# Kernel tuning notes

Hardware: AMD Instinct MI355X
Metric: run time of the kernel (lower is better)

The kernel has to match this reference:

```python
import jax, jax.numpy as jnp
import numpy as np

N_QUBITS = 10
DEPTH = 6


def _ry(theta):
    # RY(theta) = [[cos(t/2), -sin(t/2)], [sin(t/2), cos(t/2)]]
    c = jnp.cos(theta / 2)
    s = jnp.sin(theta / 2)
    return jnp.stack([jnp.stack([c, -s]), jnp.stack([s, c])]).astype(jnp.complex64)


def _rot(phi, theta, omega):
    # PennyLane Rot(phi, theta, omega) = RZ(omega) RY(theta) RZ(phi)
    c = jnp.cos(theta / 2)
    s = jnp.sin(theta / 2)
    ep = jnp.exp(-0.5j * (phi + omega).astype(jnp.complex64))
    em = jnp.exp(-0.5j * (phi - omega).astype(jnp.complex64))
    return jnp.stack([
        jnp.stack([ep * c, -jnp.conj(em) * s]),
        jnp.stack([em * s, jnp.conj(ep) * c]),
    ])


def _apply_1q(psi, U, w):
    # psi: (2,)*n statevector; apply 2x2 unitary U on qubit axis w
    psi = jnp.tensordot(U, psi, axes=([1], [w]))
    return jnp.moveaxis(psi, 0, w)


def _apply_cnot(psi, c, t):
    # flip target axis t on the control=1 slice of axis c
    psi = jnp.moveaxis(psi, (c, t), (0, 1))
    psi = jnp.concatenate([psi[:1], psi[1:, ::-1]], axis=0)
    return jnp.moveaxis(psi, (0, 1), (c, t))


def _circuit(angles, weights):
    """RY encoding + StronglyEntanglingLayers + PauliZ expvals. angles: (n,), weights: (depth, n, 3)."""
    n = N_QUBITS
    psi = jnp.zeros((2,) * n, jnp.complex64).at[(0,) * n].set(1.0)
    for i in range(n):
        psi = _apply_1q(psi, _ry(angles[i]), i)
    for l in range(DEPTH):
        for i in range(n):
            psi = _apply_1q(psi, _rot(weights[l, i, 0], weights[l, i, 1], weights[l, i, 2]), i)
        r = (l % (n - 1)) + 1  # default StronglyEntanglingLayers range schedule
        for i in range(n):
            psi = _apply_cnot(psi, i, (i + r) % n)
    p = psi.real ** 2 + psi.imag ** 2  # probabilities, shape (2,)*n
    exps = []
    for i in range(n):
        pm = jnp.moveaxis(p, i, 0).reshape(2, -1).sum(axis=1)
        exps.append(pm[0] - pm[1])  # <Z_i>
    return jnp.stack(exps)


def setup_inputs() -> dict:
    key = jax.random.key(0)
    ks = jax.random.split(key, 5)
    B, F, C = 8192, 1024, 10
    x = jax.random.normal(ks[0], (B, F), jnp.float32)
    W_proj = jax.random.normal(ks[1], (N_QUBITS, F), jnp.float32) / np.sqrt(F).astype(np.float32)
    weights = 0.01 * jax.random.normal(ks[2], (DEPTH, N_QUBITS, 3), jnp.float32)
    W_out = jax.random.normal(ks[3], (C, N_QUBITS), jnp.float32) / np.sqrt(N_QUBITS).astype(np.float32)
    b_out = 0.01 * jax.random.normal(ks[4], (C,), jnp.float32)
    return {"x": x, "W_proj": W_proj, "weights": weights, "W_out": W_out, "b_out": b_out}


def reference(x, W_proj, weights, W_out, b_out):
    # classical projection + angle encoding
    angles = jnp.tanh(x @ W_proj.T) * jnp.float32(np.pi / 2)  # (B, n_qubits)
    # batched exact statevector simulation of the VQC
    q = jax.vmap(_circuit, in_axes=(0, None))(angles, weights)  # (B, n_qubits)
    return q @ W_out.T + b_out  # (B, num_classes)
```

## Files before the change

kernel.cpp:

```cpp
#include <hip/hip_runtime.h>
#include <math.h>
#include <stdint.h>

#define NQ 10
#define DEPTH 6

typedef _Float16 f16x8 __attribute__((ext_vector_type(8)));
typedef float f32x4 __attribute__((ext_vector_type(4)));

typedef __attribute__((address_space(3))) unsigned int lds_u32;
typedef const __attribute__((address_space(1))) unsigned int glb_u32;

__device__ __forceinline__ void async_load16(const unsigned short* g, unsigned short* l) {
    __builtin_amdgcn_global_load_lds((glb_u32*)g, (lds_u32*)l, 16, 0, 0);
}

template <int M>
__device__ __forceinline__ float lane_xor(float v) {
    if constexpr (M == 1) {
        int r = __builtin_amdgcn_update_dpp(
            __builtin_bit_cast(int, v), __builtin_bit_cast(int, v),
            0xB1, 0xF, 0xF, false);
        return __builtin_bit_cast(float, r);
    } else if constexpr (M == 2) {
        int r = __builtin_amdgcn_update_dpp(
            __builtin_bit_cast(int, v), __builtin_bit_cast(int, v),
            0x4E, 0xF, 0xF, false);
        return __builtin_bit_cast(float, r);
    } else if constexpr (M == 4) {
        return __builtin_bit_cast(float,
            __builtin_amdgcn_ds_swizzle(__builtin_bit_cast(int, v), 0x101F));
    } else if constexpr (M == 8) {
        return __builtin_bit_cast(float,
            __builtin_amdgcn_ds_swizzle(__builtin_bit_cast(int, v), 0x201F));
    } else if constexpr (M == 16) {
        return __builtin_bit_cast(float,
            __builtin_amdgcn_ds_swizzle(__builtin_bit_cast(int, v), 0x401F));
    } else {
        return __shfl_xor(v, 32, 64);
    }
}

__device__ __forceinline__ void compute_gate(const float* __restrict__ weights,
                                             int idx, float* __restrict__ g) {
    float phi   = weights[idx * 3 + 0];
    float theta = weights[idx * 3 + 1];
    float omega = weights[idx * 3 + 2];
    float c = cosf(0.5f * theta), s = sinf(0.5f * theta);
    float ap = -0.5f * (phi + omega);
    float am = -0.5f * (phi - omega);
    float epr = cosf(ap), epi = sinf(ap);
    float emr = cosf(am), emi = sinf(am);
    g[0] =  epr * c;  g[1] =  epi * c;
    g[2] = -emr * s;  g[3] =  emi * s;
    g[4] =  emr * s;  g[5] =  emi * s;
    g[6] =  epr * c;  g[7] = -epi * c;
}

__global__ void prep_gates_kernel(const float* __restrict__ weights,
                                  float* __restrict__ gmat) {
    int idx = blockIdx.x * blockDim.x + threadIdx.x;
    if (idx >= DEPTH * NQ) return;
    compute_gate(weights, idx, gmat + idx * 8);
}

template <int Q>
__device__ __forceinline__ void rotT_gate(float (&ar)[16], float (&ai)[16], int lane,
                                          const float* __restrict__ g) {
    float u00r = g[0], u00i = g[1];
    float u01r = g[4], u01i = g[5];
    float u10r = g[2], u10i = g[3];
    float u11r = g[6], u11i = g[7];
    if constexpr (Q < 4) {
#pragma unroll
        for (int j = 0; j < 16; ++j) {
            if ((j >> Q) & 1) continue;
            int j1 = j | (1 << Q);
            float a0r = ar[j],  a0i = ai[j];
            float a1r = ar[j1], a1i = ai[j1];
            ar[j]  = u00r*a0r - u00i*a0i + u01r*a1r - u01i*a1i;
            ai[j]  = u00r*a0i + u00i*a0r + u01r*a1i + u01i*a1r;
            ar[j1] = u10r*a0r - u10i*a0i + u11r*a1r - u11i*a1i;
            ai[j1] = u10r*a0i + u10i*a0r + u11r*a1i + u11i*a1r;
        }
    } else {
        constexpr int M = 1 << (Q - 4);
        bool hi = (lane >> (Q - 4)) & 1;
        float car = hi ? u11r : u00r, cai = hi ? u11i : u00i;
        float cbr = hi ? u10r : u01r, cbi = hi ? u10i : u01i;
        float pr[16], pi[16];
#pragma unroll
        for (int j = 0; j < 16; ++j) pr[j] = lane_xor<M>(ar[j]);
#pragma unroll
        for (int j = 0; j < 16; ++j) pi[j] = lane_xor<M>(ai[j]);
#pragma unroll
        for (int j = 0; j < 16; ++j) {
            float mr = ar[j], mi = ai[j];
            ar[j] = car*mr - cai*mi + cbr*pr[j] - cbi*pi[j];
            ai[j] = car*mi + cai*mr + cbr*pi[j] + cbi*pr[j];
        }
    }
}

__device__ __forceinline__ void rotT_layer(float (&ar)[16], float (&ai)[16], int lane,
                                           const float* __restrict__ gl) {
    rotT_gate<0>(ar, ai, lane, gl + 0);
    rotT_gate<1>(ar, ai, lane, gl + 8);
    rotT_gate<2>(ar, ai, lane, gl + 16);
    rotT_gate<3>(ar, ai, lane, gl + 24);
    rotT_gate<4>(ar, ai, lane, gl + 32);
    rotT_gate<5>(ar, ai, lane, gl + 40);
    rotT_gate<6>(ar, ai, lane, gl + 48);
    rotT_gate<7>(ar, ai, lane, gl + 56);
    rotT_gate<8>(ar, ai, lane, gl + 64);
    rotT_gate<9>(ar, ai, lane, gl + 72);
}

template <int C, int T>
__device__ __forceinline__ void cnot_t(float (&ar)[16], float (&ai)[16], int lane) {
    if constexpr (C < 4 && T < 4) {
#pragma unroll
        for (int j = 0; j < 16; ++j) {
            if (((j >> C) & 1) && !((j >> T) & 1)) {
                int j1 = j | (1 << T);
                float tr = ar[j]; ar[j] = ar[j1]; ar[j1] = tr;
                float ti = ai[j]; ai[j] = ai[j1]; ai[j1] = ti;
            }
        }
    } else if constexpr (C < 4) {
        constexpr int M = 1 << (T - 4);
        float pr[16], pi[16];
#pragma unroll
        for (int j = 0; j < 16; ++j)
            if ((j >> C) & 1) pr[j] = lane_xor<M>(ar[j]);
#pragma unroll
        for (int j = 0; j < 16; ++j)
            if ((j >> C) & 1) pi[j] = lane_xor<M>(ai[j]);
#pragma unroll
        for (int j = 0; j < 16; ++j)
            if ((j >> C) & 1) { ar[j] = pr[j]; ai[j] = pi[j]; }
    } else if constexpr (T < 4) {
        bool cb = (lane >> (C - 4)) & 1;
#pragma unroll
        for (int j = 0; j < 16; ++j) {
            if (!((j >> T) & 1)) {
                int j1 = j | (1 << T);
                float lr = ar[j], li = ai[j], hr = ar[j1], hi2 = ai[j1];
                ar[j]  = cb ? hr : lr;  ai[j]  = cb ? hi2 : li;
                ar[j1] = cb ? lr : hr;  ai[j1] = cb ? li : hi2;
            }
        }
    } else {
        constexpr int M = 1 << (T - 4);
        bool cb = (lane >> (C - 4)) & 1;
        float pr[16], pi[16];
#pragma unroll
        for (int j = 0; j < 16; ++j) pr[j] = lane_xor<M>(ar[j]);
#pragma unroll
        for (int j = 0; j < 16; ++j) pi[j] = lane_xor<M>(ai[j]);
#pragma unroll
        for (int j = 0; j < 16; ++j) {
            ar[j] = cb ? pr[j] : ar[j];
            ai[j] = cb ? pi[j] : ai[j];
        }
    }
}

template <int R, int I>
__device__ __forceinline__ void cnot_ring_rev_t(float (&ar)[16], float (&ai)[16], int lane) {
    cnot_t<I, (I + R) % NQ>(ar, ai, lane);
    if constexpr (I > 0) cnot_ring_rev_t<R, I - 1>(ar, ai, lane);
}

__device__ __forceinline__ void run_circuit_T(float (&ar)[16], float (&ai)[16],
                                              const float* __restrict__ gmat, int lane) {
    for (int l = DEPTH - 1; l >= 0; --l) {
        switch (l) {
            case 0: cnot_ring_rev_t<1, NQ - 1>(ar, ai, lane); break;
            case 1: cnot_ring_rev_t<2, NQ - 1>(ar, ai, lane); break;
            case 2: cnot_ring_rev_t<3, NQ - 1>(ar, ai, lane); break;
            case 3: cnot_ring_rev_t<4, NQ - 1>(ar, ai, lane); break;
            case 4: cnot_ring_rev_t<5, NQ - 1>(ar, ai, lane); break;
            default: cnot_ring_rev_t<6, NQ - 1>(ar, ai, lane); break;
        }
        rotT_layer(ar, ai, lane, gmat + l * (NQ * 8));
    }
}

__device__ __forceinline__ float wave_sum(float v) {
    v += lane_xor<1>(v);
    v += lane_xor<2>(v);
    v += lane_xor<4>(v);
    v += lane_xor<8>(v);
    v += lane_xor<16>(v);
    v += lane_xor<32>(v);
    return v;
}

__device__ __forceinline__ void apply_1q_local(
    float (&ar)[16], float (&ai)[16], int q,
    float u00r, float u00i, float u01r, float u01i,
    float u10r, float u10i, float u11r, float u11i) {
#pragma unroll
    for (int j = 0; j < 16; ++j) {
        if ((j >> q) & 1) continue;
        int j1 = j | (1 << q);
        float a0r = ar[j],  a0i = ai[j];
        float a1r = ar[j1], a1i = ai[j1];
        ar[j]  = u00r*a0r - u00i*a0i + u01r*a1r - u01i*a1i;
        ai[j]  = u00r*a0i + u00i*a0r + u01r*a1i + u01i*a1r;
        ar[j1] = u10r*a0r - u10i*a0i + u11r*a1r - u11i*a1i;
        ai[j1] = u10r*a0i + u10i*a0r + u11r*a1i + u11i*a1r;
    }
}

__device__ __forceinline__ void apply_1q_lane(
    float (&ar)[16], float (&ai)[16], int q, int lane,
    float u00r, float u00i, float u01r, float u01i,
    float u10r, float u10i, float u11r, float u11i) {
    int  m  = 1 << (q - 4);
    bool hi = (lane >> (q - 4)) & 1;
    float car = hi ? u11r : u00r, cai = hi ? u11i : u00i;
    float cbr = hi ? u10r : u01r, cbi = hi ? u10i : u01i;
    float pr[16], pi[16];
#pragma unroll
    for (int j = 0; j < 16; ++j) pr[j] = __shfl_xor(ar[j], m, 64);
#pragma unroll
    for (int j = 0; j < 16; ++j) pi[j] = __shfl_xor(ai[j], m, 64);
#pragma unroll
    for (int j = 0; j < 16; ++j) {
        float mr = ar[j], mi = ai[j];
        ar[j] = car*mr - cai*mi + cbr*pr[j] - cbi*pi[j];
        ai[j] = car*mi + cai*mr + cbr*pi[j] + cbi*pr[j];
    }
}

__device__ __forceinline__ void cnot_gate(
    float (&ar)[16], float (&ai)[16], int c, int t, int lane) {
    if (c < 4 && t < 4) {
#pragma unroll
        for (int j = 0; j < 16; ++j) {
            if (((j >> c) & 1) && !((j >> t) & 1)) {
                int j1 = j | (1 << t);
                float tr = ar[j]; ar[j] = ar[j1]; ar[j1] = tr;
                float ti = ai[j]; ai[j] = ai[j1]; ai[j1] = ti;
            }
        }
    } else if (c < 4) {
        int m = 1 << (t - 4);
        float pr[16], pi[16];
#pragma unroll
        for (int j = 0; j < 16; ++j)
            if ((j >> c) & 1) pr[j] = __shfl_xor(ar[j], m, 64);
#pragma unroll
        for (int j = 0; j < 16; ++j)
            if ((j >> c) & 1) pi[j] = __shfl_xor(ai[j], m, 64);
#pragma unroll
        for (int j = 0; j < 16; ++j)
            if ((j >> c) & 1) { ar[j] = pr[j]; ai[j] = pi[j]; }
    } else if (t < 4) {
        bool cb = (lane >> (c - 4)) & 1;
#pragma unroll
        for (int j = 0; j < 16; ++j) {
            if (!((j >> t) & 1)) {
                int j1 = j | (1 << t);
                float lr = ar[j], li = ai[j], hr = ar[j1], hi2 = ai[j1];
                ar[j]  = cb ? hr : lr;  ai[j]  = cb ? hi2 : li;
                ar[j1] = cb ? lr : hr;  ai[j1] = cb ? li : hi2;
            }
        }
    } else {
        int  m  = 1 << (t - 4);
        bool cb = (lane >> (c - 4)) & 1;
        float pr[16], pi[16];
#pragma unroll
        for (int j = 0; j < 16; ++j) pr[j] = __shfl_xor(ar[j], m, 64);
#pragma unroll
        for (int j = 0; j < 16; ++j) pi[j] = __shfl_xor(ai[j], m, 64);
#pragma unroll
        for (int j = 0; j < 16; ++j) {
            ar[j] = cb ? pr[j] : ar[j];
            ai[j] = cb ? pi[j] : ai[j];
        }
    }
}

template <int R>
__device__ __forceinline__ void cnot_ring(float (&ar)[16], float (&ai)[16], int lane) {
#pragma unroll
    for (int i = 0; i < NQ; ++i) cnot_gate(ar, ai, i, (i + R) % NQ, lane);
}

__device__ __forceinline__ void run_circuit(float (&ar)[16], float (&ai)[16],
                                            const float* __restrict__ gmat, int lane) {
    for (int l = 0; l < DEPTH; ++l) {
        const float* gl = gmat + l * (NQ * 8);
#pragma unroll
        for (int i = 0; i < NQ; ++i) {
            const float* g = gl + i * 8;
            float u00r = g[0], u00i = g[1], u01r = g[2], u01i = g[3];
            float u10r = g[4], u10i = g[5], u11r = g[6], u11i = g[7];
            if (i < 4)
                apply_1q_local(ar, ai, i, u00r,u00i,u01r,u01i,u10r,u10i,u11r,u11i);
            else
                apply_1q_lane(ar, ai, i, lane, u00r,u00i,u01r,u01i,u10r,u10i,u11r,u11i);
        }
        switch (l) {
            case 0: cnot_ring<1>(ar, ai, lane); break;
            case 1: cnot_ring<2>(ar, ai, lane); break;
            case 2: cnot_ring<3>(ar, ai, lane); break;
            case 3: cnot_ring<4>(ar, ai, lane); break;
            case 4: cnot_ring<5>(ar, ai, lane); break;
            default: cnot_ring<6>(ar, ai, lane); break;
        }
    }
}

__device__ __forceinline__ void proj_v_body(
    const float* __restrict__ x, const float* __restrict__ Wproj,
    _Float16* __restrict__ V, int b, int lane) {
    const float4* xb4 = (const float4*)(x + (size_t)b * 1024);
    const float4* W4  = (const float4*)Wproj;
    float acc[NQ];
#pragma unroll
    for (int q = 0; q < NQ; ++q) acc[q] = 0.f;
#pragma unroll
    for (int k4 = 0; k4 < 4; ++k4) {
        float4 xv = xb4[k4 * 64 + lane];
#pragma unroll
        for (int q = 0; q < NQ; ++q) {
            float4 wv = W4[q * 256 + k4 * 64 + lane];
            acc[q] = fmaf(xv.x, wv.x, acc[q]);
            acc[q] = fmaf(xv.y, wv.y, acc[q]);
            acc[q] = fmaf(xv.z, wv.z, acc[q]);
            acc[q] = fmaf(xv.w, wv.w, acc[q]);
        }
    }
#pragma unroll
    for (int q = 0; q < NQ; ++q) acc[q] = wave_sum(acc[q]);

    float cq[NQ], sq[NQ];
#pragma unroll
    for (int q = 0; q < NQ; ++q) {
        float e  = __expf(2.f * acc[q]);
        float th = 1.f - __fdividef(2.f, e + 1.f);
        float ha = th * 0.785398163397448310f;
        cq[q] = __cosf(ha);
        sq[q] = __sinf(ha);
    }
    float laneprod = 1.f;
#pragma unroll
    for (int q = 4; q < NQ; ++q)
        laneprod *= ((lane >> (q - 4)) & 1) ? sq[q] : cq[q];

    unsigned int buf[8];
#pragma unroll
    for (int jj = 0; jj < 8; ++jj) {
        unsigned short h2[2];
#pragma unroll
        for (int c = 0; c < 2; ++c) {
            int j = jj * 2 + c;
            float p = laneprod;
#pragma unroll
            for (int q = 0; q < 4; ++q) p *= ((j >> q) & 1) ? sq[q] : cq[q];
            h2[c] = __builtin_bit_cast(unsigned short, (_Float16)p);
        }
        buf[jj] = (unsigned int)h2[0] | ((unsigned int)h2[1] << 16);
    }
    uint4* dst = (uint4*)(V + (size_t)b * 1024 + 16 * lane);
    uint4 v0; v0.x = buf[0]; v0.y = buf[1]; v0.z = buf[2]; v0.w = buf[3];
    uint4 v1; v1.x = buf[4]; v1.y = buf[5]; v1.z = buf[6]; v1.w = buf[7];
    dst[0] = v0; dst[1] = v1;
}

__global__ __launch_bounds__(256) void basis_proj_kernel(
    const float* __restrict__ weights, _Float16* __restrict__ Bt,
    const float* __restrict__ x, const float* __restrict__ Wproj,
    _Float16* __restrict__ V, int B) {
    __shared__ float gmat_s[DEPTH * NQ * 8];
    int tid  = threadIdx.x;
    int lane = tid & 63;
    int w    = tid >> 6;

    if (blockIdx.x < 256) {
        if (tid < DEPTH * NQ) compute_gate(weights, tid, gmat_s + tid * 8);
        __syncthreads();

        int g = blockIdx.x * 4 + w;
        float ar[16], ai[16];
#pragma unroll
        for (int jj = 0; jj < 16; ++jj) {
            ar[jj] = (lane == (g >> 4) && jj == (g & 15)) ? 1.f : 0.f;
            ai[jj] = 0.f;
        }
        run_circuit_T(ar, ai, gmat_s, lane);

        unsigned int bufr[8], bufi[8];
#pragma unroll
        for (int jj = 0; jj < 8; ++jj) {
            unsigned short r0 = __builtin_bit_cast(unsigned short, (_Float16)ar[2*jj]);
            unsigned short r1 = __builtin_bit_cast(unsigned short, (_Float16)ar[2*jj+1]);
            unsigned short i0 = __builtin_bit_cast(unsigned short, (_Float16)ai[2*jj]);
            unsigned short i1 = __builtin_bit_cast(unsigned short, (_Float16)ai[2*jj+1]);
            bufr[jj] = (unsigned int)r0 | ((unsigned int)r1 << 16);
            bufi[jj] = (unsigned int)i0 | ((unsigned int)i1 << 16);
        }
        uint4* dre = (uint4*)((unsigned short*)Bt + (size_t)(2*g)     * 1024 + 16 * lane);
        uint4* dim = (uint4*)((unsigned short*)Bt + (size_t)(2*g + 1) * 1024 + 16 * lane);
        uint4 v;
        v.x = bufr[0]; v.y = bufr[1]; v.z = bufr[2]; v.w = bufr[3]; dre[0] = v;
        v.x = bufr[4]; v.y = bufr[5]; v.z = bufr[6]; v.w = bufr[7]; dre[1] = v;
        v.x = bufi[0]; v.y = bufi[1]; v.z = bufi[2]; v.w = bufi[3]; dim[0] = v;
        v.x = bufi[4]; v.y = bufi[5]; v.z = bufi[6]; v.w = bufi[7]; dim[1] = v;
    } else {
        int b = (blockIdx.x - 256) * 4 + w;
        if (b < B) proj_v_body(x, Wproj, V, b, lane);
    }
}

#define STG(dst_, src_, kt_) do {                                                   \
    _Pragma("unroll")                                                               \
    for (int s_ = 0; s_ < 2; ++s_) {                                                \
        async_load16(src_ + (size_t)(s_ * 128 + srow) * 1024 + (kt_) * 32 + scg * 8,\
                     dst_ + s_ * 4096 + w * 512);                                   \
    }                                                                               \
} while (0)

__global__ __launch_bounds__(512, 2) void gemm_fused_kernel(
    const unsigned short* __restrict__ A,
    const unsigned short* __restrict__ Bt,
    float* __restrict__ Zpart) {
    __shared__ __align__(16) unsigned short lds_s[4 * 16384];
    int tid  = threadIdx.x;
    int lane = tid & 63;
    int w    = tid >> 6;
    int wm   = w >> 2;
    int wn   = w & 3;
    int by   = blockIdx.x & 7;
    int bx   = blockIdx.x >> 3;
    int m0   = bx * 256;
    int n0   = by * 256;
    int quad = lane >> 4;
    int lrow = lane & 15;
    int csw  = (quad ^ ((lrow >> 1) & 3)) * 8;
    int srow = tid >> 2;
    int scg  = (tid & 3) ^ ((srow >> 1) & 3);
    const unsigned short* Abase = A  + (size_t)m0 * 1024;
    const unsigned short* Bbase = Bt + (size_t)n0 * 1024;

    f32x4 acc[8][4];
#pragma unroll
    for (int mi = 0; mi < 8; ++mi)
#pragma unroll
        for (int ni = 0; ni < 4; ++ni)
            acc[mi][ni] = (f32x4){0.f, 0.f, 0.f, 0.f};

    STG(lds_s + 0 * 16384,        Abase, 0);
    STG(lds_s + 0 * 16384 + 8192, Bbase, 0);
    STG(lds_s + 1 * 16384,        Abase, 1);
    STG(lds_s + 1 * 16384 + 8192, Bbase, 1);
    STG(lds_s + 2 * 16384,        Abase, 2);
    STG(lds_s + 2 * 16384 + 8192, Bbase, 2);
    asm volatile("s_waitcnt vmcnt(8)" ::: "memory");
    __builtin_amdgcn_s_barrier();

    int rowA = wm * 128 + lrow;
    int rowB = wn * 64  + lrow;

    for (int t = 0; t < 32; ++t) {
        const unsigned short* bufA = lds_s + (t & 3) * 16384;
        const unsigned short* bufB = bufA + 8192;
        unsigned short* nbuf = lds_s + ((t + 3) & 3) * 16384;
        f16x8 af[4], bf[4];
#pragma unroll
        for (int i = 0; i < 4; ++i)
            af[i] = *(const f16x8*)(bufA + (rowA + i * 16) * 32 + csw);
#pragma unroll
        for (int i = 0; i < 4; ++i)
            bf[i] = *(const f16x8*)(bufB + (rowB + i * 16) * 32 + csw);
        if (t < 29) STG(nbuf, Abase, t + 3);
        __builtin_amdgcn_s_barrier();
        asm volatile("s_waitcnt lgkmcnt(0)" ::: "memory");
        __builtin_amdgcn_sched_barrier(0);
        __builtin_amdgcn_s_setprio(1);
#pragma unroll
        for (int mi = 0; mi < 4; ++mi)
#pragma unroll
            for (int ni = 0; ni < 4; ++ni)
                acc[mi][ni] = __builtin_amdgcn_mfma_f32_16x16x32_f16(
                    af[mi], bf[ni], acc[mi][ni], 0, 0, 0);
        __builtin_amdgcn_s_setprio(0);
        __builtin_amdgcn_s_barrier();
#pragma unroll
        for (int i = 0; i < 4; ++i)
            af[i] = *(const f16x8*)(bufA + (rowA + 64 + i * 16) * 32 + csw);
        if (t < 29) {
            STG(nbuf + 8192, Bbase, t + 3);
            asm volatile("s_waitcnt vmcnt(8)" ::: "memory");
        } else {
            asm volatile("s_waitcnt vmcnt(0)" ::: "memory");
        }
        __builtin_amdgcn_s_barrier();
        asm volatile("s_waitcnt lgkmcnt(0)" ::: "memory");
        __builtin_amdgcn_sched_barrier(0);
        __builtin_amdgcn_s_setprio(1);
#pragma unroll
        for (int mi = 0; mi < 4; ++mi)
#pragma unroll
            for (int ni = 0; ni < 4; ++ni)
                acc[mi + 4][ni] = __builtin_amdgcn_mfma_f32_16x16x32_f16(
                    af[mi], bf[ni], acc[mi + 4][ni], 0, 0, 0);
        __builtin_amdgcn_s_setprio(0);
        __builtin_amdgcn_s_barrier();
    }

    float* Zs = (float*)lds_s;
    int nbl  = wn >> 1;
    int half = wn & 1;
#pragma unroll
    for (int mi = 0; mi < 8; ++mi) {
#pragma unroll
        for (int r = 0; r < 4; ++r) {
            float p0 = acc[mi][0][r] * acc[mi][0][r];
            float p1 = acc[mi][1][r] * acc[mi][1][r];
            float p2 = acc[mi][2][r] * acc[mi][2][r];
            float p3 = acc[mi][3][r] * acc[mi][3][r];
            float t0 = (p0 + p1) + (p2 + p3);
            float t3 = (p0 - p1) + (p2 - p3);
            float t4 = (p0 + p1) - (p2 + p3);
            t0 += lane_xor<1>(t0);
            t3 += lane_xor<1>(t3);
            t4 += lane_xor<1>(t4);
            float u2 = lane_xor<2>(t0);
            float ap = t0 + u2;
            float am = (lane & 2) ? u2 - t0 : t0 - u2;
            t3 += lane_xor<2>(t3);
            t4 += lane_xor<2>(t4);
            float u4  = lane_xor<4>(ap);
            float bpp = ap + u4;
            float bpm = (lane & 4) ? u4 - ap : ap - u4;
            float bmp = am + lane_xor<4>(am);
            t3 += lane_xor<4>(t3);
            t4 += lane_xor<4>(t4);
            float u8 = lane_xor<8>(bpp);
            float T  = bpp + u8;
            float Z2 = (lane & 8) ? u8 - bpp : bpp - u8;
            float Z1 = bpm + lane_xor<8>(bpm);
            float Z0 = bmp + lane_xor<8>(bmp);
            t3 += lane_xor<8>(t3);
            t4 += lane_xor<8>(t4);
            if (lrow == 0) {
                int row = wm * 128 + mi * 16 + quad * 4 + r;
                float* z = Zs + ((size_t)(nbl * 2 + half) * 256 + row) * 9;
                z[0] = T;  z[1] = Z0; z[2] = Z1; z[3] = Z2;
                z[4] = t3; z[5] = t4;
            }
        }
    }
    __syncthreads();
    {
        int row  = tid >> 1, part = tid & 1;
#pragma unroll
        for (int nb = 0; nb < 2; ++nb) {
            const float* za = Zs + ((size_t)(nb * 2 + 0) * 256 + row) * 9;
            const float* zb = Zs + ((size_t)(nb * 2 + 1) * 256 + row) * 9;
            float o[4];
            if (part == 0) {
                o[0] = za[0] + zb[0];
                o[1] = za[1] + zb[1];
                o[2] = za[2] + zb[2];
                o[3] = za[3] + zb[3];
            } else {
                o[0] = za[4] + zb[4];
                o[1] = za[5] + zb[5];
                o[2] = za[0] - zb[0];
                o[3] = 0.f;
            }
            float4 v = {o[0], o[1], o[2], o[3]};
            *(float4*)(Zpart + ((size_t)(m0 + row) * 16 + (by * 2 + nb)) * 8 + part * 4) = v;
        }
    }
}

__global__ __launch_bounds__(256) void combine_head_kernel(
    const float* __restrict__ Zpart, const float* __restrict__ Wout,
    const float* __restrict__ bout, float* __restrict__ out, int B) {
    int lane = threadIdx.x & 63;
    int wid  = threadIdx.x >> 6;
    int b    = blockIdx.x * 4 + wid;
    if (b >= B) return;

    float z[8];
    if (lane < 16) {
        const float4* p = (const float4*)(Zpart + ((size_t)b * 16 + lane) * 8);
        float4 a = p[0], c = p[1];
        z[0]=a.x; z[1]=a.y; z[2]=a.z; z[3]=a.w; z[4]=c.x; z[5]=c.y; z[6]=c.z; z[7]=c.w;
    } else {
#pragma unroll
        for (int i = 0; i < 8; ++i) z[i] = 0.f;
    }
    float Zq[NQ];
#pragma unroll
    for (int q = 0; q < 6; ++q) {
        float v = z[q + 1];
        v += lane_xor<1>(v);
        v += lane_xor<2>(v);
        v += lane_xor<4>(v);
        v += lane_xor<8>(v);
        Zq[q] = v;
    }
    {
        float T = z[0];
        float u1 = lane_xor<1>(T);
        float P  = T + u1;
        float M  = (lane & 1) ? u1 - T : T - u1;
        float u2 = lane_xor<2>(P);
        float PP = P + u2;
        float PM = (lane & 2) ? u2 - P : P - u2;
        float MP = M + lane_xor<2>(M);
        float u4  = lane_xor<4>(PP);
        float PPP = PP + u4;
        float PPM = (lane & 4) ? u4 - PP : PP - u4;
        float PMP = PM + lane_xor<4>(PM);
        float MPP = MP + lane_xor<4>(MP);
        float u8 = lane_xor<8>(PPP);
        Zq[9] = (lane & 8) ? u8 - PPP : PPP - u8;
        Zq[8] = PPM + lane_xor<8>(PPM);
        Zq[7] = PMP + lane_xor<8>(PMP);
        Zq[6] = MPP + lane_xor<8>(MPP);
    }
    if (lane < NQ) {
        float o = bout[lane];
#pragma unroll
        for (int q = 0; q < NQ; ++q) o = fmaf(Zq[q], Wout[lane * NQ + q], o);
        out[(size_t)b * NQ + lane] = o;
    }
}

__global__ __launch_bounds__(256) void vqc_kernel(
    const float* __restrict__ x, const float* __restrict__ Wproj,
    const float* __restrict__ gmat, const float* __restrict__ Wout,
    const float* __restrict__ bout, float* __restrict__ out, int B) {
    int lane = threadIdx.x & 63;
    int wid  = threadIdx.x >> 6;
    int b    = blockIdx.x * 4 + wid;
    if (b >= B) return;

    const float* xb = x + (size_t)b * 1024;
    float acc[NQ];
#pragma unroll
    for (int q = 0; q < NQ; ++q) acc[q] = 0.f;
#pragma unroll
    for (int k = 0; k < 16; ++k) {
        float xv = xb[k * 64 + lane];
#pragma unroll
        for (int q = 0; q < NQ; ++q)
            acc[q] = fmaf(xv, Wproj[q * 1024 + k * 64 + lane], acc[q]);
    }
#pragma unroll
    for (int q = 0; q < NQ; ++q) acc[q] = wave_sum(acc[q]);

    float cq[NQ], sq[NQ];
#pragma unroll
    for (int q = 0; q < NQ; ++q) {
        float ang = tanhf(acc[q]) * 1.57079632679489662f;
        cq[q] = cosf(0.5f * ang);
        sq[q] = sinf(0.5f * ang);
    }
    float laneprod = 1.f;
#pragma unroll
    for (int q = 4; q < NQ; ++q)
        laneprod *= ((lane >> (q - 4)) & 1) ? sq[q] : cq[q];
    float ar[16], ai[16];
#pragma unroll
    for (int j = 0; j < 16; ++j) {
        float p = laneprod;
#pragma unroll
        for (int q = 0; q < 4; ++q) p *= ((j >> q) & 1) ? sq[q] : cq[q];
        ar[j] = p; ai[j] = 0.f;
    }
    run_circuit(ar, ai, gmat, lane);

    float T = 0.f, S[4] = {0.f, 0.f, 0.f, 0.f};
#pragma unroll
    for (int j = 0; j < 16; ++j) {
        float p = ar[j] * ar[j] + ai[j] * ai[j];
        T += p;
#pragma unroll
        for (int q = 0; q < 4; ++q) S[q] += ((j >> q) & 1) ? -p : p;
    }
    float Zq[NQ];
#pragma unroll
    for (int q = 0; q < 4; ++q) Zq[q] = S[q];
#pragma unroll
    for (int q = 4; q < NQ; ++q) Zq[q] = ((lane >> (q - 4)) & 1) ? -T : T;
#pragma unroll
    for (int q = 0; q < NQ; ++q) Zq[q] = wave_sum(Zq[q]);
    if (lane < NQ) {
        float o = bout[lane];
#pragma unroll
        for (int q = 0; q < NQ; ++q) o = fmaf(Zq[q], Wout[lane * NQ + q], o);
        out[(size_t)b * NQ + lane] = o;
    }
}

extern "C" void kernel_launch(void* const* d_in, const int* in_sizes, int n_in,
                              void* d_out, int out_size, void* d_ws, size_t ws_size,
                              hipStream_t stream) {
    const float* x       = (const float*)d_in[0];
    const float* Wproj   = (const float*)d_in[1];
    const float* weights = (const float*)d_in[2];
    const float* Wout    = (const float*)d_in[3];
    const float* bout    = (const float*)d_in[4];
    float* out = (float*)d_out;
    int B = in_sizes[0] / 1024;

    char* ws = (char*)d_ws;
    size_t off_Bt = 4096;
    size_t off_V  = off_Bt + (size_t)2048 * 1024 * 2;
    size_t off_Z  = off_V  + (size_t)B * 1024 * 2;
    size_t need   = off_Z  + (size_t)B * 16 * 8 * 4;

    if (ws_size >= need && (B % 256) == 0) {
        _Float16* Bt = (_Float16*)(ws + off_Bt);
        _Float16* V  = (_Float16*)(ws + off_V);
        float*  Zprt = (float*)(ws + off_Z);

        basis_proj_kernel<<<256 + B / 4, 256, 0, stream>>>(weights, Bt, x, Wproj, V, B);
        gemm_fused_kernel<<<(B / 256) * 8, 512, 0, stream>>>(
            (const unsigned short*)V, (const unsigned short*)Bt, Zprt);
        combine_head_kernel<<<B / 4, 256, 0, stream>>>(Zprt, Wout, bout, out, B);
    } else {
        float* gmat = (float*)ws;
        prep_gates_kernel<<<1, 64, 0, stream>>>(weights, gmat);
        vqc_kernel<<<(B + 3) / 4, 256, 0, stream>>>(x, Wproj, gmat, Wout, bout, out, B);
    }
}
```

Measured before the change: 149.6 us.

## Fuse combine/head stage into GEMM epilogue with atomic accumulation into output

Removes the separate combine_head kernel and the Zpart workspace. Each GEMM block now folds its partial per-qubit expectation sums through W_out and atomically adds them into the output, with the bias added by the by==0 blocks. The output is zeroed in the basis/projection kernel, which also moves to 512-thread blocks. This drops one launch and the partial-sum round trip through global memory. The cost is 10 float atomics per row per column block and a non-deterministic summation order.

```diff
diff --git a/kernel.cpp b/kernel.cpp
--- a/kernel.cpp
+++ b/kernel.cpp
@@ -373,20 +373,22 @@
     dst[0] = v0; dst[1] = v1;
 }
 
-__global__ __launch_bounds__(256) void basis_proj_kernel(
+__global__ __launch_bounds__(512) void basis_proj_kernel(
     const float* __restrict__ weights, _Float16* __restrict__ Bt,
     const float* __restrict__ x, const float* __restrict__ Wproj,
-    _Float16* __restrict__ V, int B) {
+    _Float16* __restrict__ V, float* __restrict__ out, int B) {
     __shared__ float gmat_s[DEPTH * NQ * 8];
     int tid  = threadIdx.x;
     int lane = tid & 63;
     int w    = tid >> 6;
 
-    if (blockIdx.x < 256) {
+    if (blockIdx.x < 128) {
+        for (int i = blockIdx.x * 512 + tid; i < B * NQ; i += 128 * 512)
+            out[i] = 0.f;
         if (tid < DEPTH * NQ) compute_gate(weights, tid, gmat_s + tid * 8);
         __syncthreads();
 
-        int g = blockIdx.x * 4 + w;
+        int g = blockIdx.x * 8 + w;
         float ar[16], ai[16];
 #pragma unroll
         for (int jj = 0; jj < 16; ++jj) {
@@ -413,7 +415,7 @@
         v.x = bufi[0]; v.y = bufi[1]; v.z = bufi[2]; v.w = bufi[3]; dim[0] = v;
         v.x = bufi[4]; v.y = bufi[5]; v.z = bufi[6]; v.w = bufi[7]; dim[1] = v;
     } else {
-        int b = (blockIdx.x - 256) * 4 + w;
+        int b = (int)(blockIdx.x - 128) * 8 + w;
         if (b < B) proj_v_body(x, Wproj, V, b, lane);
     }
 }
@@ -429,7 +431,9 @@
 __global__ __launch_bounds__(512, 2) void gemm_fused_kernel(
     const unsigned short* __restrict__ A,
     const unsigned short* __restrict__ Bt,
-    float* __restrict__ Zpart) {
+    const float* __restrict__ Wout,
+    const float* __restrict__ bout,
+    float* __restrict__ out) {
     __shared__ __align__(16) unsigned short lds_s[4 * 16384];
     int tid  = threadIdx.x;
     int lane = tid & 63;
@@ -558,82 +562,37 @@
         }
     }
     __syncthreads();
-    {
-        int row  = tid >> 1, part = tid & 1;
-#pragma unroll
-        for (int nb = 0; nb < 2; ++nb) {
-            const float* za = Zs + ((size_t)(nb * 2 + 0) * 256 + row) * 9;
-            const float* zb = Zs + ((size_t)(nb * 2 + 1) * 256 + row) * 9;
-            float o[4];
-            if (part == 0) {
-                o[0] = za[0] + zb[0];
-                o[1] = za[1] + zb[1];
-                o[2] = za[2] + zb[2];
-                o[3] = za[3] + zb[3];
-            } else {
-                o[0] = za[4] + zb[4];
-                o[1] = za[5] + zb[5];
-                o[2] = za[0] - zb[0];
-                o[3] = 0.f;
-            }
-            float4 v = {o[0], o[1], o[2], o[3]};
-            *(float4*)(Zpart + ((size_t)(m0 + row) * 16 + (by * 2 + nb)) * 8 + part * 4) = v;
-        }
-    }
-}
-
-__global__ __launch_bounds__(256) void combine_head_kernel(
-    const float* __restrict__ Zpart, const float* __restrict__ Wout,
-    const float* __restrict__ bout, float* __restrict__ out, int B) {
-    int lane = threadIdx.x & 63;
-    int wid  = threadIdx.x >> 6;
-    int b    = blockIdx.x * 4 + wid;
-    if (b >= B) return;
-
-    float z[8];
-    if (lane < 16) {
-        const float4* p = (const float4*)(Zpart + ((size_t)b * 16 + lane) * 8);
-        float4 a = p[0], c = p[1];
-        z[0]=a.x; z[1]=a.y; z[2]=a.z; z[3]=a.w; z[4]=c.x; z[5]=c.y; z[6]=c.z; z[7]=c.w;
-    } else {
-#pragma unroll
-        for (int i = 0; i < 8; ++i) z[i] = 0.f;
-    }
-    float Zq[NQ];
-#pragma unroll
-    for (int q = 0; q < 6; ++q) {
-        float v = z[q + 1];
-        v += lane_xor<1>(v);
-        v += lane_xor<2>(v);
-        v += lane_xor<4>(v);
-        v += lane_xor<8>(v);
-        Zq[q] = v;
-    }
-    {
-        float T = z[0];
-        float u1 = lane_xor<1>(T);
-        float P  = T + u1;
-        float M  = (lane & 1) ? u1 - T : T - u1;
-        float u2 = lane_xor<2>(P);
-        float PP = P + u2;
-        float PM = (lane & 2) ? u2 - P : P - u2;
-        float MP = M + lane_xor<2>(M);
-        float u4  = lane_xor<4>(PP);
-        float PPP = PP + u4;
-        float PPM = (lane & 4) ? u4 - PP : PP - u4;
-        float PMP = PM + lane_xor<4>(PM);
-        float MPP = MP + lane_xor<4>(MP);
-        float u8 = lane_xor<8>(PPP);
-        Zq[9] = (lane & 8) ? u8 - PPP : PPP - u8;
-        Zq[8] = PPM + lane_xor<8>(PPM);
-        Zq[7] = PMP + lane_xor<8>(PMP);
-        Zq[6] = MPP + lane_xor<8>(MPP);
-    }
-    if (lane < NQ) {
-        float o = bout[lane];
-#pragma unroll
-        for (int q = 0; q < NQ; ++q) o = fmaf(Zq[q], Wout[lane * NQ + q], o);
-        out[(size_t)b * NQ + lane] = o;
+    if (tid < 256) {
+        int row = tid;
+        float contrib[NQ];
+#pragma unroll
+        for (int q = 0; q < NQ; ++q) contrib[q] = 0.f;
+#pragma unroll
+        for (int nbl2 = 0; nbl2 < 2; ++nbl2) {
+            const float* za = Zs + ((size_t)(nbl2 * 2 + 0) * 256 + row) * 9;
+            const float* zb = Zs + ((size_t)(nbl2 * 2 + 1) * 256 + row) * 9;
+            float Ta = za[0], Tb = zb[0];
+            contrib[0] += za[1] + zb[1];
+            contrib[1] += za[2] + zb[2];
+            contrib[2] += za[3] + zb[3];
+            contrib[3] += za[4] + zb[4];
+            contrib[4] += za[5] + zb[5];
+            contrib[5] += Ta - Tb;
+            float Tnb = Ta + Tb;
+            int nb = by * 2 + nbl2;
+            contrib[6] += (nb & 1) ? -Tnb : Tnb;
+            contrib[7] += (nb & 2) ? -Tnb : Tnb;
+            contrib[8] += (nb & 4) ? -Tnb : Tnb;
+            contrib[9] += (nb & 8) ? -Tnb : Tnb;
+        }
+        float* orow = out + (size_t)(m0 + row) * NQ;
+#pragma unroll
+        for (int c = 0; c < NQ; ++c) {
+            float o = (by == 0) ? bout[c] : 0.f;
+#pragma unroll
+            for (int q = 0; q < NQ; ++q) o = fmaf(contrib[q], Wout[c * NQ + q], o);
+            atomicAdd(&orow[c], o);
+        }
     }
 }
 
@@ -718,18 +677,15 @@
     char* ws = (char*)d_ws;
     size_t off_Bt = 4096;
     size_t off_V  = off_Bt + (size_t)2048 * 1024 * 2;
-    size_t off_Z  = off_V  + (size_t)B * 1024 * 2;
-    size_t need   = off_Z  + (size_t)B * 16 * 8 * 4;
+    size_t need   = off_V  + (size_t)B * 1024 * 2;
 
     if (ws_size >= need && (B % 256) == 0) {
         _Float16* Bt = (_Float16*)(ws + off_Bt);
         _Float16* V  = (_Float16*)(ws + off_V);
-        float*  Zprt = (float*)(ws + off_Z);
-
-        basis_proj_kernel<<<256 + B / 4, 256, 0, stream>>>(weights, Bt, x, Wproj, V, B);
+
+        basis_proj_kernel<<<128 + B / 8, 512, 0, stream>>>(weights, Bt, x, Wproj, V, out, B);
         gemm_fused_kernel<<<(B / 256) * 8, 512, 0, stream>>>(
-            (const unsigned short*)V, (const unsigned short*)Bt, Zprt);
-        combine_head_kernel<<<B / 4, 256, 0, stream>>>(Zprt, Wout, bout, out, B);
+            (const unsigned short*)V, (const unsigned short*)Bt, Wout, bout, out);
     } else {
         float* gmat = (float*)ws;
         prep_gates_kernel<<<1, 64, 0, stream>>>(weights, gmat);
```

Result: slower. 168.7 us (+12.7%).

## Halve GEMM M-tile to 128 with double-buffered LDS and higher occupancy

Applied to the files above, without the earlier changes.

The fused GEMM tile shrinks from 256x256 to 128x256, so each block does one MFMA phase per k-step instead of two. The 4-stage LDS ring becomes a 2-buffer double-buffer, which cuts LDS to 48 KB per block. Launch bounds rise to allow 4 blocks per CU, and the grid doubles so each CU holds more resident blocks. The aim is better latency hiding and load balance across CUs. In exchange it gives up the deeper prefetch pipeline and reloads the B tile more often, and it waits with vmcnt(0) every iteration.

```diff
diff --git a/kernel.cpp b/kernel.cpp
--- a/kernel.cpp
+++ b/kernel.cpp
@@ -418,19 +418,21 @@
     }
 }
 
-#define STG(dst_, src_, kt_) do {                                                   \
+#define STG(dstA_, dstB_, kt_) do {                                                 \
+    async_load16(Abase + (size_t)srow * 1024 + (kt_) * 32 + scg * 8,                \
+                 dstA_ + w * 512);                                                  \
     _Pragma("unroll")                                                               \
     for (int s_ = 0; s_ < 2; ++s_) {                                                \
-        async_load16(src_ + (size_t)(s_ * 128 + srow) * 1024 + (kt_) * 32 + scg * 8,\
-                     dst_ + s_ * 4096 + w * 512);                                   \
+        async_load16(Bbase + (size_t)(s_ * 128 + srow) * 1024 + (kt_) * 32 + scg * 8,\
+                     dstB_ + s_ * 4096 + w * 512);                                  \
     }                                                                               \
 } while (0)
 
-__global__ __launch_bounds__(512, 2) void gemm_fused_kernel(
+__global__ __launch_bounds__(512, 4) void gemm_fused_kernel(
     const unsigned short* __restrict__ A,
     const unsigned short* __restrict__ Bt,
     float* __restrict__ Zpart) {
-    __shared__ __align__(16) unsigned short lds_s[4 * 16384];
+    __shared__ __align__(16) unsigned short lds_s[2 * 12288];
     int tid  = threadIdx.x;
     int lane = tid & 63;
     int w    = tid >> 6;
@@ -438,7 +440,7 @@
     int wn   = w & 3;
     int by   = blockIdx.x & 7;
     int bx   = blockIdx.x >> 3;
-    int m0   = bx * 256;
+    int m0   = bx * 128;
     int n0   = by * 256;
     int quad = lane >> 4;
     int lrow = lane & 15;
@@ -448,29 +450,25 @@
     const unsigned short* Abase = A  + (size_t)m0 * 1024;
     const unsigned short* Bbase = Bt + (size_t)n0 * 1024;
 
-    f32x4 acc[8][4];
-#pragma unroll
-    for (int mi = 0; mi < 8; ++mi)
+    f32x4 acc[4][4];
+#pragma unroll
+    for (int mi = 0; mi < 4; ++mi)
 #pragma unroll
         for (int ni = 0; ni < 4; ++ni)
             acc[mi][ni] = (f32x4){0.f, 0.f, 0.f, 0.f};
 
-    STG(lds_s + 0 * 16384,        Abase, 0);
-    STG(lds_s + 0 * 16384 + 8192, Bbase, 0);
-    STG(lds_s + 1 * 16384,        Abase, 1);
-    STG(lds_s + 1 * 16384 + 8192, Bbase, 1);
-    STG(lds_s + 2 * 16384,        Abase, 2);
-    STG(lds_s + 2 * 16384 + 8192, Bbase, 2);
-    asm volatile("s_waitcnt vmcnt(8)" ::: "memory");
+    STG(lds_s, lds_s + 4096, 0);
+    asm volatile("s_waitcnt vmcnt(0)" ::: "memory");
     __builtin_amdgcn_s_barrier();
 
-    int rowA = wm * 128 + lrow;
-    int rowB = wn * 64  + lrow;
+    int rowA = wm * 64 + lrow;
+    int rowB = wn * 64 + lrow;
 
     for (int t = 0; t < 32; ++t) {
-        const unsigned short* bufA = lds_s + (t & 3) * 16384;
-        const unsigned short* bufB = bufA + 8192;
-        unsigned short* nbuf = lds_s + ((t + 3) & 3) * 16384;
+        const unsigned short* bufA = lds_s + (t & 1) * 12288;
+        const unsigned short* bufB = bufA + 4096;
+        unsigned short* nA = lds_s + ((t + 1) & 1) * 12288;
+        if (t < 31) STG(nA, nA + 4096, t + 1);
         f16x8 af[4], bf[4];
 #pragma unroll
         for (int i = 0; i < 4; ++i)
@@ -478,8 +476,6 @@
 #pragma unroll
         for (int i = 0; i < 4; ++i)
             bf[i] = *(const f16x8*)(bufB + (rowB + i * 16) * 32 + csw);
-        if (t < 29) STG(nbuf, Abase, t + 3);
-        __builtin_amdgcn_s_barrier();
         asm volatile("s_waitcnt lgkmcnt(0)" ::: "memory");
         __builtin_amdgcn_sched_barrier(0);
         __builtin_amdgcn_s_setprio(1);
@@ -490,27 +486,7 @@
                 acc[mi][ni] = __builtin_amdgcn_mfma_f32_16x16x32_f16(
                     af[mi], bf[ni], acc[mi][ni], 0, 0, 0);
         __builtin_amdgcn_s_setprio(0);
-        __builtin_amdgcn_s_barrier();
-#pragma unroll
-        for (int i = 0; i < 4; ++i)
-            af[i] = *(const f16x8*)(bufA + (rowA + 64 + i * 16) * 32 + csw);
-        if (t < 29) {
-            STG(nbuf + 8192, Bbase, t + 3);
-            asm volatile("s_waitcnt vmcnt(8)" ::: "memory");
-        } else {
-            asm volatile("s_waitcnt vmcnt(0)" ::: "memory");
-        }
-        __builtin_amdgcn_s_barrier();
-        asm volatile("s_waitcnt lgkmcnt(0)" ::: "memory");
-        __builtin_amdgcn_sched_barrier(0);
-        __builtin_amdgcn_s_setprio(1);
-#pragma unroll
-        for (int mi = 0; mi < 4; ++mi)
-#pragma unroll
-            for (int ni = 0; ni < 4; ++ni)
-                acc[mi + 4][ni] = __builtin_amdgcn_mfma_f32_16x16x32_f16(
-                    af[mi], bf[ni], acc[mi + 4][ni], 0, 0, 0);
-        __builtin_amdgcn_s_setprio(0);
+        asm volatile("s_waitcnt vmcnt(0)" ::: "memory");
         __builtin_amdgcn_s_barrier();
     }
 
@@ -518,7 +494,7 @@
     int nbl  = wn >> 1;
     int half = wn & 1;
 #pragma unroll
-    for (int mi = 0; mi < 8; ++mi) {
+    for (int mi = 0; mi < 4; ++mi) {
 #pragma unroll
         for (int r = 0; r < 4; ++r) {
             float p0 = acc[mi][0][r] * acc[mi][0][r];
@@ -550,8 +526,8 @@
             t3 += lane_xor<8>(t3);
             t4 += lane_xor<8>(t4);
             if (lrow == 0) {
-                int row = wm * 128 + mi * 16 + quad * 4 + r;
-                float* z = Zs + ((size_t)(nbl * 2 + half) * 256 + row) * 9;
+                int row = wm * 64 + mi * 16 + quad * 4 + r;
+                float* z = Zs + ((size_t)(nbl * 2 + half) * 128 + row) * 9;
                 z[0] = T;  z[1] = Z0; z[2] = Z1; z[3] = Z2;
                 z[4] = t3; z[5] = t4;
             }
@@ -559,26 +535,25 @@
     }
     __syncthreads();
     {
-        int row  = tid >> 1, part = tid & 1;
-#pragma unroll
-        for (int nb = 0; nb < 2; ++nb) {
-            const float* za = Zs + ((size_t)(nb * 2 + 0) * 256 + row) * 9;
-            const float* zb = Zs + ((size_t)(nb * 2 + 1) * 256 + row) * 9;
-            float o[4];
-            if (part == 0) {
-                o[0] = za[0] + zb[0];
-                o[1] = za[1] + zb[1];
-                o[2] = za[2] + zb[2];
-                o[3] = za[3] + zb[3];
-            } else {
-                o[0] = za[4] + zb[4];
-                o[1] = za[5] + zb[5];
-                o[2] = za[0] - zb[0];
-                o[3] = 0.f;
-            }
-            float4 v = {o[0], o[1], o[2], o[3]};
-            *(float4*)(Zpart + ((size_t)(m0 + row) * 16 + (by * 2 + nb)) * 8 + part * 4) = v;
-        }
+        int row  = tid >> 2;
+        int nb   = (tid >> 1) & 1;
+        int part = tid & 1;
+        const float* za = Zs + ((size_t)(nb * 2 + 0) * 128 + row) * 9;
+        const float* zb = Zs + ((size_t)(nb * 2 + 1) * 128 + row) * 9;
+        float o[4];
+        if (part == 0) {
+            o[0] = za[0] + zb[0];
+            o[1] = za[1] + zb[1];
+            o[2] = za[2] + zb[2];
+            o[3] = za[3] + zb[3];
+        } else {
+            o[0] = za[4] + zb[4];
+            o[1] = za[5] + zb[5];
+            o[2] = za[0] - zb[0];
+            o[3] = 0.f;
+        }
+        float4 v = {o[0], o[1], o[2], o[3]};
+        *(float4*)(Zpart + ((size_t)(m0 + row) * 16 + (by * 2 + nb)) * 8 + part * 4) = v;
     }
 }
 
@@ -721,15 +696,15 @@
     size_t off_Z  = off_V  + (size_t)B * 1024 * 2;
     size_t need   = off_Z  + (size_t)B * 16 * 8 * 4;
 
-    if (ws_size >= need && (B % 256) == 0) {
+    if (ws_size >= need && (B % 128) == 0) {
         _Float16* Bt = (_Float16*)(ws + off_Bt);
         _Float16* V  = (_Float16*)(ws + off_V);
         float*  Zprt = (float*)(ws + off_Z);
 
-        basis_proj_kernel<<<256 + B / 4, 256, 0, stream>>>(weights, Bt, x, Wproj, V, B);
-        gemm_fused_kernel<<<(B / 256) * 8, 512, 0, stream>>>(
+        basis_proj_kernel<<<256 + (B + 3) / 4, 256, 0, stream>>>(weights, Bt, x, Wproj, V, B);
+        gemm_fused_kernel<<<(B / 128) * 8, 512, 0, stream>>>(
             (const unsigned short*)V, (const unsigned short*)Bt, Zprt);
-        combine_head_kernel<<<B / 4, 256, 0, stream>>>(Zprt, Wout, bout, out, B);
+        combine_head_kernel<<<(B + 3) / 4, 256, 0, stream>>>(Zprt, Wout, bout, out, B);
     } else {
         float* gmat = (float*)ws;
         prep_gates_kernel<<<1, 64, 0, stream>>>(weights, gmat);
```

Measured after the change: 143.6 us, median of 2. 1.04x faster.
